# Optimization experiments

Measured on AMD Instinct MI355X. Metric: run time of the kernel, lower is better.

## Reference

```python
import jax, jax.numpy as jnp
import numpy as np

IN_C = 64
OUT_C = 128
HEADS = 8
DIM = 9 * IN_C  # 576


def unfold3x3_s2(fea):
    # torch.nn.functional.unfold(fea, (3,3), padding=1, stride=2)
    # returns [N, C*9, L] with channel-major (c, kh, kw) ordering.
    N, C, H, W = fea.shape
    Ho, Wo = H // 2, W // 2
    p = jnp.pad(fea, ((0, 0), (0, 0), (1, 1), (1, 1)))
    patches = jnp.stack(
        [p[:, :, ki:ki + 2 * Ho:2, kj:kj + 2 * Wo:2] for ki in range(3) for kj in range(3)],
        axis=2,
    )  # [N, C, 9, Ho, Wo]
    return patches.reshape(N, C * 9, Ho * Wo)


def mhsa(x, w_qkv, b_qkv, w_out, b_out):
    # standard ViT attention: x [B, L, D]
    B, L, D = x.shape
    dh = D // HEADS
    qkv = x @ w_qkv + b_qkv  # [B, L, 3D]
    q, k, v = jnp.split(qkv, 3, axis=-1)
    def heads(t):
        return t.reshape(B, L, HEADS, dh).transpose(0, 2, 1, 3)  # [B, h, L, dh]
    q, k, v = heads(q), heads(k), heads(v)
    scale = dh ** -0.5
    scores = jnp.einsum('bhqd,bhkd->bhqk', q, k) * scale
    attn = jax.nn.softmax(scores, axis=-1)
    o = jnp.einsum('bhqk,bhkd->bhqd', attn, v)  # [B, h, L, dh]
    o = o.transpose(0, 2, 1, 3).reshape(B, L, D)
    return o @ w_out + b_out


def setup_inputs() -> dict:
    key = jax.random.key(0)
    ks = jax.random.split(key, 6)
    s = DIM ** -0.5
    return {
        'fea': jax.random.normal(ks[0], (1, IN_C, 128, 128), dtype=jnp.float32),
        'w_qkv': jax.random.normal(ks[1], (DIM, 3 * DIM), dtype=jnp.float32) * s,
        'b_qkv': jnp.zeros((3 * DIM,), dtype=jnp.float32),
        'w_out': jax.random.normal(ks[2], (DIM, DIM), dtype=jnp.float32) * s,
        'b_out': jnp.zeros((DIM,), dtype=jnp.float32),
        'conv_w': jax.random.normal(ks[3], (OUT_C, IN_C, 3, 3), dtype=jnp.float32) * s,
    }


def reference(fea, w_qkv, b_qkv, w_out, b_out, conv_w):
    N, C, H, W = fea.shape
    Ho, Wo = H // 2, W // 2
    x = unfold3x3_s2(fea).transpose(0, 2, 1)          # [N, L, 9C]
    x = mhsa(x, w_qkv, b_qkv, w_out, b_out) + x       # residual
    # matmul with reshaped conv weights: [N, L, 9C] @ [9C, out_c]
    y = x @ conv_w.reshape(OUT_C, -1).T               # [N, L, out_c]
    y = y.transpose(0, 2, 1).reshape(N, OUT_C, Ho, Wo)  # fold with (1,1) kernel
    return jax.nn.silu(y)
```

## Files before the change

### kernel.cpp

```cpp
#include <hip/hip_runtime.h>
#include <hip/hip_bf16.h>
#include <math.h>

#define L_TOK 4096
#define D_DIM 576
#define NHEADS 8
#define DHEAD 72
#define DPAD 96
#define HSZ ((size_t)NHEADS * L_TOK * DPAD)
#define KSPLIT 4
#define LOG2E 1.4426950408889634f
#define SCALE2 (0.11785113019775792f * 1.4426950408889634f)

typedef __attribute__((ext_vector_type(8))) short short8;
typedef __attribute__((ext_vector_type(4))) short short4v;
typedef __attribute__((ext_vector_type(4))) float float4v;

union F4S8 {
  float4 f4;
  short8 s8;
  __hip_bfloat16 h[8];
};

__device__ inline void tc_body(const float* __restrict__ src,
                               __hip_bfloat16* __restrict__ dst, int R, int C,
                               int bi, int bj, int t, __hip_bfloat16* Ts) {
  const int col = t & 63, row4 = t >> 6;
#pragma unroll
  for (int u = 0; u < 16; u++) {
    int r = u * 4 + row4;
    Ts[r * 68 + col] = __float2bfloat16(src[(size_t)(bj * 64 + r) * C + bi * 64 + col]);
  }
  __syncthreads();
#pragma unroll
  for (int u = 0; u < 16; u++) {
    int c = u * 4 + row4;
    dst[(size_t)(bi * 64 + c) * R + bj * 64 + col] = Ts[col * 68 + c];
  }
}

__global__ __launch_bounds__(256) void prep_all(const float* __restrict__ fea,
                                                const float* __restrict__ w_qkv,
                                                const float* __restrict__ w_out,
                                                const float* __restrict__ conv_w,
                                                __hip_bfloat16* __restrict__ xb,
                                                __hip_bfloat16* __restrict__ WqkvT,
                                                __hip_bfloat16* __restrict__ WoT,
                                                __hip_bfloat16* __restrict__ CwB) {
  __shared__ float Shm[3120];
  const int b = blockIdx.x;
  const int t = threadIdx.x;
  if (b < 512) {
    float* Lf = Shm;
    const int ho = b & 63;
    const int c0 = (b >> 6) * 8;
    for (int e = t; e < 3072; e += 256) {
      int c = e / 384;
      int rr = (e / 128) % 3;
      int w = e & 127;
      int h = 2 * ho + rr - 1;
      float v = 0.f;
      if ((unsigned)h < 128u) v = fea[(size_t)(c0 + c) * 16384 + h * 128 + w];
      Lf[(c * 3 + rr) * 130 + w + 1] = v;
    }
    if (t < 24) { Lf[t * 130] = 0.f; Lf[t * 130 + 129] = 0.f; }
    __syncthreads();
    for (int e = t; e < 576; e += 256) {
      int wo = e / 9, ch = e - wo * 9;
      F4S8 u;
#pragma unroll
      for (int j = 0; j < 8; j++) {
        int dd = ch * 8 + j;
        int c = dd / 9, k = dd - c * 9;
        int ki = k / 3, kj = k - ki * 3;
        u.h[j] = __float2bfloat16(Lf[(c * 3 + ki) * 130 + 2 * wo + kj]);
      }
      *(float4*)(xb + (size_t)(ho * 64 + wo) * D_DIM + c0 * 9 + ch * 8) = u.f4;
    }
  } else if (b < 755) {
    int bb = b - 512;
    tc_body(w_qkv, WqkvT, D_DIM, 1728, bb % 27, bb / 27, t, (__hip_bfloat16*)Shm);
  } else if (b < 836) {
    int bb = b - 755;
    tc_body(w_out, WoT, D_DIM, D_DIM, bb % 9, bb / 9, t, (__hip_bfloat16*)Shm);
  } else {
    int i = (b - 836) * 256 + t;
    CwB[i] = __float2bfloat16(conv_w[i]);
  }
}

template <int EPI, int NMI>
__global__ __launch_bounds__(256) void gemm_mfma(const __hip_bfloat16* __restrict__ A,
                                                 const __hip_bfloat16* __restrict__ Bt,
                                                 const float* __restrict__ bias,
                                                 const __hip_bfloat16* __restrict__ resid,
                                                 __hip_bfloat16* __restrict__ outB,
                                                 __hip_bfloat16* __restrict__ outB2) {
  constexpr int K = D_DIM;
  constexpr int BM = NMI * 32;
  __shared__ __align__(16) __hip_bfloat16 As[BM * 72];
  __shared__ __align__(16) __hip_bfloat16 Bs[64 * 72];
  const int t = threadIdx.x;
  const int wave = t >> 6, lane = t & 63, quad = lane >> 4, l16 = lane & 15;
  const int wm = (wave & 2) * (NMI * 8);
  const int wn = (wave & 1) * 32;
  const int m0 = blockIdx.x * BM, n0 = blockIdx.y * 64;

  float4v acc[NMI][2];
#pragma unroll
  for (int i = 0; i < NMI; i++)
#pragma unroll
    for (int j = 0; j < 2; j++) acc[i][j] = (float4v){0.f, 0.f, 0.f, 0.f};

  const int arow = t >> 3, ach = t & 7;
  for (int k0 = 0; k0 < K; k0 += 64) {
    __syncthreads();
#pragma unroll
    for (int u = 0; u < NMI; u++) {
      int row = u * 32 + arow;
      *(float4*)(&As[row * 72 + ach * 8]) =
          *(const float4*)(A + (size_t)(m0 + row) * K + k0 + ach * 8);
    }
#pragma unroll
    for (int u = 0; u < 2; u++) {
      int row = u * 32 + arow;
      *(float4*)(&Bs[row * 72 + ach * 8]) =
          *(const float4*)(Bt + (size_t)(n0 + row) * K + k0 + ach * 8);
    }
    __syncthreads();
    short8 af[NMI][2], bfr[2][2];
#pragma unroll
    for (int i = 0; i < NMI; i++)
#pragma unroll
      for (int s = 0; s < 2; s++)
        af[i][s] = *(const short8*)(&As[(wm + i * 16 + l16) * 72 + s * 32 + quad * 8]);
#pragma unroll
    for (int j = 0; j < 2; j++)
#pragma unroll
      for (int s = 0; s < 2; s++)
        bfr[j][s] = *(const short8*)(&Bs[(wn + j * 16 + l16) * 72 + s * 32 + quad * 8]);
#pragma unroll
    for (int i = 0; i < NMI; i++)
#pragma unroll
      for (int j = 0; j < 2; j++) {
        acc[i][j] = __builtin_amdgcn_mfma_f32_16x16x32_bf16(af[i][0], bfr[j][0], acc[i][j], 0, 0, 0);
        acc[i][j] = __builtin_amdgcn_mfma_f32_16x16x32_bf16(af[i][1], bfr[j][1], acc[i][j], 0, 0, 0);
      }
  }

  if (EPI == 0) {
    const int part = n0 / D_DIM;
    if (part < 2) {
      __hip_bfloat16* dst = outB + (size_t)part * HSZ;
      const float sc = (part == 0) ? SCALE2 : 1.f;
#pragma unroll
      for (int j = 0; j < 2; j++) {
        int ng = n0 + wn + j * 16 + l16;
        float bv = bias[ng];
        int rem = ng - part * D_DIM;
        int h = rem / DHEAD;
        int d = rem - h * DHEAD;
#pragma unroll
        for (int i = 0; i < NMI; i++) {
          int mb = m0 + wm + i * 16 + quad * 4;
#pragma unroll
          for (int r = 0; r < 4; r++)
            dst[((size_t)h * L_TOK + mb + r) * DPAD + d] =
                __float2bfloat16((acc[i][j][r] + bv) * sc);
        }
      }
    } else {
      __hip_bfloat16* Ls = As;
      __syncthreads();
      const int n0rel = n0 - 2 * D_DIM;
#pragma unroll
      for (int j = 0; j < 2; j++) {
        int nloc = wn + j * 16 + l16;
        float bv = bias[n0 + nloc];
#pragma unroll
        for (int i = 0; i < NMI; i++) {
          int mloc = wm + i * 16 + quad * 4;
#pragma unroll
          for (int r = 0; r < 4; r++)
            Ls[nloc * 136 + mloc + r] = __float2bfloat16(acc[i][j][r] + bv);
        }
      }
      __syncthreads();
      for (int e = t; e < 1024; e += 256) {
        int row = e >> 4, ch = e & 15;
        int ng = n0rel + row;
        int hh = ng / DHEAD, dd = ng - hh * DHEAD;
        *(float4*)(outB2 + ((size_t)hh * DPAD + dd) * L_TOK + m0 + ch * 8) =
            *(const float4*)(&Ls[row * 136 + ch * 8]);
      }
    }
  } else {
#pragma unroll
    for (int j = 0; j < 2; j++) {
      int ng = n0 + wn + j * 16 + l16;
      float bv = bias[ng];
#pragma unroll
      for (int i = 0; i < NMI; i++) {
        int mb = m0 + wm + i * 16 + quad * 4;
#pragma unroll
        for (int r = 0; r < 4; r++) {
          size_t idx = (size_t)(mb + r) * D_DIM + ng;
          float v = acc[i][j][r] + bv + __bfloat162float(resid[idx]);
          outB[idx] = __float2bfloat16(v);
        }
      }
    }
  }
}

__global__ __launch_bounds__(256) void final_small(const __hip_bfloat16* __restrict__ A,
                                                   const __hip_bfloat16* __restrict__ Bt,
                                                   float* __restrict__ out) {
  __shared__ __align__(16) __hip_bfloat16 As[32 * 72];
  __shared__ __align__(16) __hip_bfloat16 Bs[32 * 72];
  const int t = threadIdx.x;
  const int wave = t >> 6, lane = t & 63, quad = lane >> 4, l16 = lane & 15;
  const int wm = (wave & 2) * 8;
  const int wn = (wave & 1) * 16;
  const int m0 = blockIdx.x * 32, n0 = blockIdx.y * 32;

  float4v acc = (float4v){0.f, 0.f, 0.f, 0.f};

  const int arow = t >> 3, ach = t & 7;
  for (int k0 = 0; k0 < D_DIM; k0 += 64) {
    __syncthreads();
    *(float4*)(&As[arow * 72 + ach * 8]) =
        *(const float4*)(A + (size_t)(m0 + arow) * D_DIM + k0 + ach * 8);
    *(float4*)(&Bs[arow * 72 + ach * 8]) =
        *(const float4*)(Bt + (size_t)(n0 + arow) * D_DIM + k0 + ach * 8);
    __syncthreads();
    short8 af[2], bfr[2];
#pragma unroll
    for (int s = 0; s < 2; s++) {
      af[s] = *(const short8*)(&As[(wm + l16) * 72 + s * 32 + quad * 8]);
      bfr[s] = *(const short8*)(&Bs[(wn + l16) * 72 + s * 32 + quad * 8]);
    }
    acc = __builtin_amdgcn_mfma_f32_16x16x32_bf16(af[0], bfr[0], acc, 0, 0, 0);
    acc = __builtin_amdgcn_mfma_f32_16x16x32_bf16(af[1], bfr[1], acc, 0, 0, 0);
  }
  const int oc = n0 + wn + l16;
  const int mb = m0 + wm + quad * 4;
#pragma unroll
  for (int r = 0; r < 4; r++) {
    float v = acc[r];
    float sg = 1.f / (1.f + __expf(-v));
    out[(size_t)oc * L_TOK + mb + r] = v * sg;
  }
}

#define KS_STRIDE 104
#define VT_STRIDE 72
#define PS_STRIDE 40
#define KBUF (64 * KS_STRIDE)
#define VBUF (80 * VT_STRIDE)

__global__ __launch_bounds__(256, 3) void attn_mfma(const __hip_bfloat16* __restrict__ Qb,
                                                    const __hip_bfloat16* __restrict__ Kb,
                                                    const __hip_bfloat16* __restrict__ VbT,
                                                    __hip_bfloat16* __restrict__ Opart,
                                                    float* __restrict__ Ml) {
  __shared__ __align__(16) __hip_bfloat16 Ks[KBUF];
  __shared__ __align__(16) __hip_bfloat16 Vt[VBUF];
  __shared__ __align__(16) __hip_bfloat16 Ps[4 * 32 * PS_STRIDE];

  const int bid = blockIdx.x;
  const int h = bid & 7;
  const int rest = bid >> 3;
  const int ksp = rest & 3;
  const int qblk = rest >> 2;
  const int t = threadIdx.x;
  const int wave = t >> 6;
  const int lane = t & 63;
  const int quad = lane >> 4;
  const int l16 = lane & 15;

  const __hip_bfloat16* Qh = Qb + (size_t)h * L_TOK * DPAD;
  const __hip_bfloat16* Kh = Kb + (size_t)h * L_TOK * DPAD;
  const __hip_bfloat16* VhT = VbT + (size_t)h * DPAD * L_TOK;

  const int qbase = qblk * 128 + wave * 32;
  short8 qf[2][3];
#pragma unroll
  for (int mi = 0; mi < 2; mi++) {
#pragma unroll
    for (int s = 0; s < 3; s++) {
      if (s == 2 && quad >= 1) {
        qf[mi][s] = (short8){0, 0, 0, 0, 0, 0, 0, 0};
        if (quad == 1) qf[mi][s][0] = (short)0xC100;
      } else {
        qf[mi][s] = *(const short8*)(Qh + (size_t)(qbase + mi * 16 + l16) * DPAD + s * 32 + quad * 8);
      }
    }
  }

  const float4 zero4 = {0.f, 0.f, 0.f, 0.f};
  union { float4 f4; unsigned u[4]; } kpad, vones;
  kpad.u[0] = 0x00003F80u; kpad.u[1] = 0u; kpad.u[2] = 0u; kpad.u[3] = 0u;
  vones.u[0] = vones.u[1] = vones.u[2] = vones.u[3] = 0x3F803F80u;
  if (t < 192) {
    int row = t / 3, ch = 9 + t % 3;
    *(float4*)(&Ks[row * KS_STRIDE + ch * 8]) = (ch == 9) ? kpad.f4 : zero4;
  } else {
    int e = t - 192;
    int d = 72 + (e >> 3), ch = e & 7;
    *(float4*)(&Vt[d * VT_STRIDE + ch * 8]) = (d == 72) ? vones.f4 : zero4;
  }

  float4v Of[2][5];
#pragma unroll
  for (int mi = 0; mi < 2; mi++)
#pragma unroll
    for (int nt = 0; nt < 5; nt++) Of[mi][nt] = (float4v){0.f, 0.f, 0.f, 0.f};

  __hip_bfloat16* myPs = Ps + wave * 32 * PS_STRIDE;
  const int kstart = ksp * 1024;

  int kgo[3], klo[3], vgo[3], vlo[3];
#pragma unroll
  for (int u = 0; u < 3; u++) {
    int e = t + u * 256;
    int ee = (e < 576) ? e : 0;
    int row = ee / 9, ch = ee - row * 9;
    kgo[u] = row * (DPAD * 2) + ch * 16;
    klo[u] = row * (KS_STRIDE * 2) + ch * 16;
    int d = ee >> 3, c2 = ee & 7;
    vgo[u] = d * (L_TOK * 2) + c2 * 16;
    vlo[u] = d * (VT_STRIDE * 2) + c2 * 16;
  }
  const bool has3 = (t < 64);

  float4 krg0, krg1, krg2, vrg0, vrg1, vrg2;
  auto load_K = [&](int kbase) {
    const char* Kt_ = (const char*)(Kh + (size_t)kbase * DPAD);
    krg0 = *(const float4*)(Kt_ + kgo[0]);
    krg1 = *(const float4*)(Kt_ + kgo[1]);
    if (has3) krg2 = *(const float4*)(Kt_ + kgo[2]);
  };
  auto load_V = [&](int kbase) {
    const char* Vg_ = (const char*)(VhT + kbase);
    vrg0 = *(const float4*)(Vg_ + vgo[0]);
    vrg1 = *(const float4*)(Vg_ + vgo[1]);
    if (has3) vrg2 = *(const float4*)(Vg_ + vgo[2]);
  };
  auto stage_write = [&]() {
    *(float4*)((char*)Ks + klo[0]) = krg0;
    *(float4*)((char*)Ks + klo[1]) = krg1;
    *(float4*)((char*)Vt + vlo[0]) = vrg0;
    *(float4*)((char*)Vt + vlo[1]) = vrg1;
    if (has3) {
      *(float4*)((char*)Ks + klo[2]) = krg2;
      *(float4*)((char*)Vt + vlo[2]) = vrg2;
    }
  };

  auto compute = [&](int knext_base, bool prefetch) {
    float4v S[2][4];
    __builtin_amdgcn_s_setprio(1);
#pragma unroll
    for (int ks = 0; ks < 4; ks++) {
      float4v a0 = (float4v){0.f, 0.f, 0.f, 0.f};
      float4v a1 = a0;
#pragma unroll
      for (int s = 0; s < 3; s++) {
        short8 kf = *(const short8*)(&Ks[(ks * 16 + l16) * KS_STRIDE + s * 32 + quad * 8]);
        a0 = __builtin_amdgcn_mfma_f32_16x16x32_bf16(kf, qf[0][s], a0, 0, 0, 0);
        a1 = __builtin_amdgcn_mfma_f32_16x16x32_bf16(kf, qf[1][s], a1, 0, 0, 0);
      }
#pragma unroll
      for (int r = 0; r < 4; r++) { S[0][ks][r] = a0[r]; S[1][ks][r] = a1[r]; }
    }
    __builtin_amdgcn_s_setprio(0);

    if (prefetch) load_V(knext_base);

#pragma unroll
    for (int kstep = 0; kstep < 2; kstep++) {
#pragma unroll
      for (int mi = 0; mi < 2; mi++) {
#pragma unroll
        for (int k2 = 0; k2 < 2; k2++) {
          int ks = kstep * 2 + k2;
          union { short4v v; __hip_bfloat16 hh[4]; } pk;
#pragma unroll
          for (int r = 0; r < 4; r++)
            pk.hh[r] = __float2bfloat16(exp2f(S[mi][ks][r]));
          *(short4v*)(&myPs[(mi * 16 + l16) * PS_STRIDE + k2 * 16 + quad * 4]) = pk.v;
        }
      }
      short8 pa[2];
#pragma unroll
      for (int mi = 0; mi < 2; mi++)
        pa[mi] = *(const short8*)(&myPs[(mi * 16 + l16) * PS_STRIDE + quad * 8]);
      __builtin_amdgcn_s_setprio(1);
#pragma unroll
      for (int nt = 0; nt < 5; nt++) {
        short8 vb = *(const short8*)(&Vt[(nt * 16 + l16) * VT_STRIDE + kstep * 32 + quad * 8]);
        Of[0][nt] = __builtin_amdgcn_mfma_f32_16x16x32_bf16(pa[0], vb, Of[0][nt], 0, 0, 0);
        Of[1][nt] = __builtin_amdgcn_mfma_f32_16x16x32_bf16(pa[1], vb, Of[1][nt], 0, 0, 0);
      }
      __builtin_amdgcn_s_setprio(0);
    }
  };

  load_K(kstart);
  load_V(kstart);
  stage_write();
  __syncthreads();

  for (int kt = 0; kt < 15; kt++) {
    const int knext = kstart + (kt + 1) * 64;
    load_K(knext);
    compute(knext, true);
    __syncthreads();
    stage_write();
    __syncthreads();
  }
  compute(kstart, false);

  const size_t pb = ((size_t)ksp * NHEADS + h) * L_TOK;
#pragma unroll
  for (int mi = 0; mi < 2; mi++) {
#pragma unroll
    for (int nt = 0; nt < 5; nt++) {
      int d = nt * 16 + l16;
      if (d < DHEAD) {
#pragma unroll
        for (int r = 0; r < 4; r++) {
          int q = qbase + mi * 16 + quad * 4 + r;
          Opart[(pb + q) * 72 + d] = __float2bfloat16(Of[mi][nt][r]);
        }
      }
    }
  }
  if (l16 == 8) {
#pragma unroll
    for (int mi = 0; mi < 2; mi++) {
#pragma unroll
      for (int r = 0; r < 4; r++)
        Ml[pb + qbase + mi * 16 + quad * 4 + r] = Of[mi][4][r];
    }
  }
}

__global__ __launch_bounds__(256) void attn_merge(const __hip_bfloat16* __restrict__ Opart,
                                                  const float* __restrict__ Ml,
                                                  __hip_bfloat16* __restrict__ ob) {
  int idx = blockIdx.x * 256 + threadIdx.x;
  int h = idx / (L_TOK * 9);
  int rem = idx - h * (L_TOK * 9);
  int q = rem / 9;
  int ch = rem - q * 9;
  float denom = 0.f;
  float acc[8] = {0, 0, 0, 0, 0, 0, 0, 0};
#pragma unroll
  for (int s = 0; s < KSPLIT; s++) {
    size_t b = ((size_t)s * NHEADS + h) * L_TOK + q;
    denom += Ml[b];
    short8 o = *(const short8*)(Opart + b * 72 + ch * 8);
#pragma unroll
    for (int j = 0; j < 8; j++) {
      union { short ss; __hip_bfloat16 bb; } u;
      u.ss = o[j];
      acc[j] += __bfloat162float(u.bb);
    }
  }
  float inv = 1.f / denom;
  __hip_bfloat16* dst = ob + (size_t)q * D_DIM + h * DHEAD + ch * 8;
#pragma unroll
  for (int j = 0; j < 8; j++) dst[j] = __float2bfloat16(acc[j] * inv);
}

extern "C" void kernel_launch(void* const* d_in, const int* in_sizes, int n_in,
                              void* d_out, int out_size, void* d_ws, size_t ws_size,
                              hipStream_t stream) {
  const float* fea    = (const float*)d_in[0];
  const float* w_qkv  = (const float*)d_in[1];
  const float* b_qkv  = (const float*)d_in[2];
  const float* w_out  = (const float*)d_in[3];
  const float* b_out  = (const float*)d_in[4];
  const float* conv_w = (const float*)d_in[5];
  float* out = (float*)d_out;

  __hip_bfloat16* xb    = (__hip_bfloat16*)d_ws;
  __hip_bfloat16* WqkvT = xb + (size_t)L_TOK * D_DIM;
  __hip_bfloat16* WoT   = WqkvT + (size_t)1728 * D_DIM;
  __hip_bfloat16* CwB   = WoT + (size_t)D_DIM * D_DIM;
  __hip_bfloat16* QKb   = CwB + (size_t)128 * D_DIM;
  __hip_bfloat16* VbT   = QKb + 2 * HSZ;
  __hip_bfloat16* Opart = VbT + HSZ;
  float* Ml = (float*)(Opart + (size_t)KSPLIT * NHEADS * L_TOK * 72);
  __hip_bfloat16* ob = QKb;
  __hip_bfloat16* xr = Opart;

  prep_all<<<1124, 256, 0, stream>>>(fea, w_qkv, w_out, conv_w, xb, WqkvT, WoT, CwB);
  gemm_mfma<0, 4><<<dim3(32, 27), 256, 0, stream>>>(xb, WqkvT, b_qkv, nullptr, QKb, VbT);
  attn_mfma<<<1024, 256, 0, stream>>>(QKb, QKb + HSZ, VbT, Opart, Ml);
  attn_merge<<<1152, 256, 0, stream>>>(Opart, Ml, ob);
  gemm_mfma<1, 2><<<dim3(64, 9), 256, 0, stream>>>(ob, WoT, b_out, xb, xr, nullptr);
  final_small<<<dim3(128, 4), 256, 0, stream>>>(xr, CwB, out);
}
```

Before: 174.6 us.

## Coalesce SiLU output stores via LDS and synthesize padding fragments in registers

The final conv GEMM epilogue now stages SiLU results through shared memory, transposing them so each thread writes a contiguous float4 along the token dimension instead of scattered scalar stores. In the attention kernel, the constant padding columns of K (the softmax bias column) and the ones row of V are built directly in registers per lane, not written into shared memory and read back. This removes the initial padding stores and some LDS reads in the inner loop, but adds lane-dependent branches there and extra barriers in the GEMM epilogue.

```diff
diff --git a/kernel.cpp b/kernel.cpp
--- a/kernel.cpp
+++ b/kernel.cpp
@@ -243,14 +243,25 @@
     acc = __builtin_amdgcn_mfma_f32_16x16x32_bf16(af[0], bfr[0], acc, 0, 0, 0);
     acc = __builtin_amdgcn_mfma_f32_16x16x32_bf16(af[1], bfr[1], acc, 0, 0, 0);
   }
-  const int oc = n0 + wn + l16;
-  const int mb = m0 + wm + quad * 4;
+  float vs[4];
 #pragma unroll
   for (int r = 0; r < 4; r++) {
     float v = acc[r];
     float sg = 1.f / (1.f + __expf(-v));
-    out[(size_t)oc * L_TOK + mb + r] = v * sg;
-  }
+    vs[r] = v * sg;
+  }
+  __syncthreads();
+  float* Ls = (float*)As;
+  const int ocl_w = wn + l16;
+  const int tk_w = wm + quad * 4;
+#pragma unroll
+  for (int r = 0; r < 4; r++) Ls[ocl_w * 33 + tk_w + r] = vs[r];
+  __syncthreads();
+  const int ocl = t >> 3;
+  const int tk4 = (t & 7) * 4;
+  float4 o4 = {Ls[ocl * 33 + tk4], Ls[ocl * 33 + tk4 + 1],
+               Ls[ocl * 33 + tk4 + 2], Ls[ocl * 33 + tk4 + 3]};
+  *(float4*)(out + (size_t)(n0 + ocl) * L_TOK + m0 + tk4) = o4;
 }
 
 #define KS_STRIDE 104
@@ -298,18 +309,10 @@
     }
   }
 
-  const float4 zero4 = {0.f, 0.f, 0.f, 0.f};
-  union { float4 f4; unsigned u[4]; } kpad, vones;
-  kpad.u[0] = 0x00003F80u; kpad.u[1] = 0u; kpad.u[2] = 0u; kpad.u[3] = 0u;
-  vones.u[0] = vones.u[1] = vones.u[2] = vones.u[3] = 0x3F803F80u;
-  if (t < 192) {
-    int row = t / 3, ch = 9 + t % 3;
-    *(float4*)(&Ks[row * KS_STRIDE + ch * 8]) = (ch == 9) ? kpad.f4 : zero4;
-  } else {
-    int e = t - 192;
-    int d = 72 + (e >> 3), ch = e & 7;
-    *(float4*)(&Vt[d * VT_STRIDE + ch * 8]) = (d == 72) ? vones.f4 : zero4;
-  }
+  const short8 zero8 = (short8){0, 0, 0, 0, 0, 0, 0, 0};
+  short8 ones8;
+#pragma unroll
+  for (int j = 0; j < 8; j++) ones8[j] = (short)0x3F80;
 
   float4v Of[2][5];
 #pragma unroll
@@ -366,10 +369,21 @@
       float4v a0 = (float4v){0.f, 0.f, 0.f, 0.f};
       float4v a1 = a0;
 #pragma unroll
-      for (int s = 0; s < 3; s++) {
+      for (int s = 0; s < 2; s++) {
         short8 kf = *(const short8*)(&Ks[(ks * 16 + l16) * KS_STRIDE + s * 32 + quad * 8]);
         a0 = __builtin_amdgcn_mfma_f32_16x16x32_bf16(kf, qf[0][s], a0, 0, 0, 0);
         a1 = __builtin_amdgcn_mfma_f32_16x16x32_bf16(kf, qf[1][s], a1, 0, 0, 0);
+      }
+      {
+        short8 kf2;
+        if (quad == 0)
+          kf2 = *(const short8*)(&Ks[(ks * 16 + l16) * KS_STRIDE + 64]);
+        else if (quad == 1)
+          kf2 = (short8){(short)0x3F80, 0, 0, 0, 0, 0, 0, 0};
+        else
+          kf2 = zero8;
+        a0 = __builtin_amdgcn_mfma_f32_16x16x32_bf16(kf2, qf[0][2], a0, 0, 0, 0);
+        a1 = __builtin_amdgcn_mfma_f32_16x16x32_bf16(kf2, qf[1][2], a1, 0, 0, 0);
       }
 #pragma unroll
       for (int r = 0; r < 4; r++) { S[0][ks][r] = a0[r]; S[1][ks][r] = a1[r]; }
@@ -398,10 +412,21 @@
         pa[mi] = *(const short8*)(&myPs[(mi * 16 + l16) * PS_STRIDE + quad * 8]);
       __builtin_amdgcn_s_setprio(1);
 #pragma unroll
-      for (int nt = 0; nt < 5; nt++) {
+      for (int nt = 0; nt < 4; nt++) {
         short8 vb = *(const short8*)(&Vt[(nt * 16 + l16) * VT_STRIDE + kstep * 32 + quad * 8]);
         Of[0][nt] = __builtin_amdgcn_mfma_f32_16x16x32_bf16(pa[0], vb, Of[0][nt], 0, 0, 0);
         Of[1][nt] = __builtin_amdgcn_mfma_f32_16x16x32_bf16(pa[1], vb, Of[1][nt], 0, 0, 0);
+      }
+      {
+        short8 vb4;
+        if (l16 < 8)
+          vb4 = *(const short8*)(&Vt[(64 + l16) * VT_STRIDE + kstep * 32 + quad * 8]);
+        else if (l16 == 8)
+          vb4 = ones8;
+        else
+          vb4 = zero8;
+        Of[0][4] = __builtin_amdgcn_mfma_f32_16x16x32_bf16(pa[0], vb4, Of[0][4], 0, 0, 0);
+        Of[1][4] = __builtin_amdgcn_mfma_f32_16x16x32_bf16(pa[1], vb4, Of[1][4], 0, 0, 0);
       }
       __builtin_amdgcn_s_setprio(0);
     }
```

Measured after the change: 180.7 us. +3.5%, slower.

## Double-buffer K/V shared-memory tiles in attention and shrink padded LDS strides

Applied to the files above, without the earlier changes.

The attention kernel now keeps two LDS buffers for K and V and alternates between them, so each iteration needs one barrier instead of two. K and V strides and row counts are trimmed so the doubled buffers fit without losing occupancy. The third K chunk and the fifth V tile are read with clamped or remapped offsets, so the pad and ones columns no longer need full-width storage. The last iteration still issues a redundant prefetch and stage write into the unused buffer, and the smaller strides may change LDS bank conflicts.

```diff
diff --git a/kernel.cpp b/kernel.cpp
--- a/kernel.cpp
+++ b/kernel.cpp
@@ -253,19 +253,19 @@
   }
 }
 
-#define KS_STRIDE 104
+#define KS_STRIDE 88
 #define VT_STRIDE 72
 #define PS_STRIDE 40
 #define KBUF (64 * KS_STRIDE)
-#define VBUF (80 * VT_STRIDE)
+#define VBUF (74 * VT_STRIDE)
 
 __global__ __launch_bounds__(256, 3) void attn_mfma(const __hip_bfloat16* __restrict__ Qb,
                                                     const __hip_bfloat16* __restrict__ Kb,
                                                     const __hip_bfloat16* __restrict__ VbT,
                                                     __hip_bfloat16* __restrict__ Opart,
                                                     float* __restrict__ Ml) {
-  __shared__ __align__(16) __hip_bfloat16 Ks[KBUF];
-  __shared__ __align__(16) __hip_bfloat16 Vt[VBUF];
+  __shared__ __align__(16) __hip_bfloat16 Ks[2 * KBUF];
+  __shared__ __align__(16) __hip_bfloat16 Vt[2 * VBUF];
   __shared__ __align__(16) __hip_bfloat16 Ps[4 * 32 * PS_STRIDE];
 
   const int bid = blockIdx.x;
@@ -298,17 +298,22 @@
     }
   }
 
-  const float4 zero4 = {0.f, 0.f, 0.f, 0.f};
-  union { float4 f4; unsigned u[4]; } kpad, vones;
-  kpad.u[0] = 0x00003F80u; kpad.u[1] = 0u; kpad.u[2] = 0u; kpad.u[3] = 0u;
-  vones.u[0] = vones.u[1] = vones.u[2] = vones.u[3] = 0x3F803F80u;
-  if (t < 192) {
-    int row = t / 3, ch = 9 + t % 3;
-    *(float4*)(&Ks[row * KS_STRIDE + ch * 8]) = (ch == 9) ? kpad.f4 : zero4;
-  } else {
-    int e = t - 192;
-    int d = 72 + (e >> 3), ch = e & 7;
-    *(float4*)(&Vt[d * VT_STRIDE + ch * 8]) = (d == 72) ? vones.f4 : zero4;
+  {
+    const float4 zero4 = {0.f, 0.f, 0.f, 0.f};
+    union { float4 f4; unsigned u[4]; } kpad, vones;
+    kpad.u[0] = 0x00003F80u; kpad.u[1] = 0u; kpad.u[2] = 0u; kpad.u[3] = 0u;
+    vones.u[0] = vones.u[1] = vones.u[2] = vones.u[3] = 0x3F803F80u;
+    if (t < 128) {
+      int row = t & 63, buf = t >> 6;
+      __hip_bfloat16* B = Ks + buf * KBUF;
+      *(float4*)(&B[row * KS_STRIDE + 72]) = kpad.f4;
+      *(float4*)(&B[row * KS_STRIDE + 80]) = zero4;
+    } else if (t < 160) {
+      int e = t - 128;
+      int buf = e >> 4, r2 = (e >> 3) & 1, ch = e & 7;
+      __hip_bfloat16* B = Vt + buf * VBUF;
+      *(float4*)(&B[(72 + r2) * VT_STRIDE + ch * 8]) = r2 ? zero4 : vones.f4;
+    }
   }
 
   float4v Of[2][5];
@@ -347,18 +352,22 @@
     vrg1 = *(const float4*)(Vg_ + vgo[1]);
     if (has3) vrg2 = *(const float4*)(Vg_ + vgo[2]);
   };
-  auto stage_write = [&]() {
-    *(float4*)((char*)Ks + klo[0]) = krg0;
-    *(float4*)((char*)Ks + klo[1]) = krg1;
-    *(float4*)((char*)Vt + vlo[0]) = vrg0;
-    *(float4*)((char*)Vt + vlo[1]) = vrg1;
+  auto stage_write = [&](__hip_bfloat16* Kw, __hip_bfloat16* Vw) {
+    *(float4*)((char*)Kw + klo[0]) = krg0;
+    *(float4*)((char*)Kw + klo[1]) = krg1;
+    *(float4*)((char*)Vw + vlo[0]) = vrg0;
+    *(float4*)((char*)Vw + vlo[1]) = vrg1;
     if (has3) {
-      *(float4*)((char*)Ks + klo[2]) = krg2;
-      *(float4*)((char*)Vt + vlo[2]) = vrg2;
+      *(float4*)((char*)Kw + klo[2]) = krg2;
+      *(float4*)((char*)Vw + vlo[2]) = vrg2;
     }
   };
 
-  auto compute = [&](int knext_base, bool prefetch) {
+  auto body = [&](int kt, const __hip_bfloat16* Ksb, const __hip_bfloat16* Vtb,
+                  __hip_bfloat16* Kw, __hip_bfloat16* Vw) {
+    const int knext = (kt < 15) ? kt + 1 : 15;
+    load_K(kstart + knext * 64);
+
     float4v S[2][4];
     __builtin_amdgcn_s_setprio(1);
 #pragma unroll
@@ -366,17 +375,23 @@
       float4v a0 = (float4v){0.f, 0.f, 0.f, 0.f};
       float4v a1 = a0;
 #pragma unroll
-      for (int s = 0; s < 3; s++) {
-        short8 kf = *(const short8*)(&Ks[(ks * 16 + l16) * KS_STRIDE + s * 32 + quad * 8]);
+      for (int s = 0; s < 2; s++) {
+        short8 kf = *(const short8*)(&Ksb[(ks * 16 + l16) * KS_STRIDE + s * 32 + quad * 8]);
         a0 = __builtin_amdgcn_mfma_f32_16x16x32_bf16(kf, qf[0][s], a0, 0, 0, 0);
         a1 = __builtin_amdgcn_mfma_f32_16x16x32_bf16(kf, qf[1][s], a1, 0, 0, 0);
       }
+      {
+        int c2s = 64 + (quad < 2 ? quad * 8 : 16);
+        short8 kf2 = *(const short8*)(&Ksb[(ks * 16 + l16) * KS_STRIDE + c2s]);
+        a0 = __builtin_amdgcn_mfma_f32_16x16x32_bf16(kf2, qf[0][2], a0, 0, 0, 0);
+        a1 = __builtin_amdgcn_mfma_f32_16x16x32_bf16(kf2, qf[1][2], a1, 0, 0, 0);
+      }
 #pragma unroll
       for (int r = 0; r < 4; r++) { S[0][ks][r] = a0[r]; S[1][ks][r] = a1[r]; }
     }
     __builtin_amdgcn_s_setprio(0);
 
-    if (prefetch) load_V(knext_base);
+    load_V(kstart + knext * 64);
 
 #pragma unroll
     for (int kstep = 0; kstep < 2; kstep++) {
@@ -398,29 +413,34 @@
         pa[mi] = *(const short8*)(&myPs[(mi * 16 + l16) * PS_STRIDE + quad * 8]);
       __builtin_amdgcn_s_setprio(1);
 #pragma unroll
-      for (int nt = 0; nt < 5; nt++) {
-        short8 vb = *(const short8*)(&Vt[(nt * 16 + l16) * VT_STRIDE + kstep * 32 + quad * 8]);
+      for (int nt = 0; nt < 4; nt++) {
+        short8 vb = *(const short8*)(&Vtb[(nt * 16 + l16) * VT_STRIDE + kstep * 32 + quad * 8]);
         Of[0][nt] = __builtin_amdgcn_mfma_f32_16x16x32_bf16(pa[0], vb, Of[0][nt], 0, 0, 0);
         Of[1][nt] = __builtin_amdgcn_mfma_f32_16x16x32_bf16(pa[1], vb, Of[1][nt], 0, 0, 0);
       }
+      {
+        int vrow = 64 + l16;
+        vrow = vrow > 73 ? 73 : vrow;
+        short8 vb4 = *(const short8*)(&Vtb[vrow * VT_STRIDE + kstep * 32 + quad * 8]);
+        Of[0][4] = __builtin_amdgcn_mfma_f32_16x16x32_bf16(pa[0], vb4, Of[0][4], 0, 0, 0);
+        Of[1][4] = __builtin_amdgcn_mfma_f32_16x16x32_bf16(pa[1], vb4, Of[1][4], 0, 0, 0);
+      }
       __builtin_amdgcn_s_setprio(0);
     }
+
+    stage_write(Kw, Vw);
+    __syncthreads();
   };
 
   load_K(kstart);
   load_V(kstart);
-  stage_write();
+  stage_write(Ks, Vt);
   __syncthreads();
 
-  for (int kt = 0; kt < 15; kt++) {
-    const int knext = kstart + (kt + 1) * 64;
-    load_K(knext);
-    compute(knext, true);
-    __syncthreads();
-    stage_write();
-    __syncthreads();
-  }
-  compute(kstart, false);
+  for (int kt2 = 0; kt2 < 16; kt2 += 2) {
+    body(kt2,     Ks,        Vt,        Ks + KBUF, Vt + VBUF);
+    body(kt2 + 1, Ks + KBUF, Vt + VBUF, Ks,        Vt);
+  }
 
   const size_t pb = ((size_t)ksp * NHEADS + h) * L_TOK;
 #pragma unroll
```

After: 179.1 us. +2.6%, slower.
